# Kernel optimization log

Measured on AMD Instinct MI355X. Metric: run time of the kernel, lower is better.

## Reference

```python
import jax, jax.numpy as jnp
import numpy as np

POINT_ENCODING_SIZE = 15
L = 0


def _bilinear_2x2(corners, R):
    """Bilinear upsample [C,2,2,F] corner grid to [C,R,R,F], align_corners=True.
    Matches F.interpolate(x, size=(R,R), mode='bilinear', align_corners=True)
    for a 2x2 spatial input.
    """
    u = jnp.linspace(0.0, 1.0, R, dtype=corners.dtype)
    wu = jnp.stack([1.0 - u, u], axis=-1)  # [R,2] weights along one axis
    return jnp.einsum('ia,jb,cabf->cijf', wu, wu, corners)


def setup_inputs() -> dict:
    key = jax.random.key(0)
    ks = jax.random.split(key, 10)
    V, C, R = 10000, 2048, 16
    points = jax.random.normal(ks[0], (V, 3), dtype=jnp.float32)
    encodings = jax.random.normal(ks[1], (V, POINT_ENCODING_SIZE), dtype=jnp.float32) * 0.1
    complexes = jax.random.randint(ks[2], (C, 4), 0, V, dtype=jnp.int64)
    d_in = POINT_ENCODING_SIZE + (L + 1) * 3  # 18
    W1 = jax.random.normal(ks[3], (128, d_in), dtype=jnp.float32) / np.sqrt(d_in)
    b1 = jax.random.normal(ks[4], (128,), dtype=jnp.float32) * 0.01
    W2 = jax.random.normal(ks[5], (128, 128), dtype=jnp.float32) / np.sqrt(128)
    b2 = jax.random.normal(ks[6], (128,), dtype=jnp.float32) * 0.01
    W3 = jax.random.normal(ks[7], (3, 128), dtype=jnp.float32) / np.sqrt(128)
    b3 = jax.random.normal(ks[8], (3,), dtype=jnp.float32) * 0.01
    return {"points": points, "encodings": encodings,
            "W1": W1, "b1": b1, "W2": W2, "b2": b2, "W3": W3, "b3": b3,
            "complexes": complexes, "resolution": R}


def reference(points, encodings, W1, b1, W2, b2, W3, b3, complexes, resolution):
    R = resolution
    # gather 4 corner vertices per complex -> [C,2,2,*]
    local_points = points[complexes].reshape(-1, 2, 2, 3)
    local_enc = encodings[complexes].reshape(-1, 2, 2, POINT_ENCODING_SIZE)
    p = _bilinear_2x2(local_points, R)   # [C,R,R,3]
    e = _bilinear_2x2(local_enc, R)      # [C,R,R,15]
    # features: encodings + sin(2^i * p), L=0 -> just sin(p)
    X = jnp.concatenate([e, jnp.sin(p)], axis=-1)  # [C,R,R,18]
    X = jnp.sin(X @ W1.T + b1)
    X = jnp.sin(X @ W2.T + b2)
    X = X @ W3.T + b3                    # [C,R,R,3]
    lipschitz = jnp.float32(1.0)
    return (p + X, X, lipschitz)
```

## Files before the change

### kernel.cpp

```cpp
#include <hip/hip_runtime.h>
#include <hip/hip_bf16.h>

#define ENC 15

typedef __attribute__((ext_vector_type(4))) float f32x4;
typedef __attribute__((ext_vector_type(8))) short s16x8;
typedef __attribute__((ext_vector_type(4))) short s16x4;

static __device__ __forceinline__ short f2bf(float v) {
    __hip_bfloat16 h = __float2bfloat16(v);
    return __builtin_bit_cast(short, h);
}

#define WAVE_FENCE() do { \
    asm volatile("s_waitcnt lgkmcnt(0)" ::: "memory"); \
    __builtin_amdgcn_sched_barrier(0); \
} while (0)

__global__ void NSC_prep_kernel(const float* __restrict__ W1,
                                const float* __restrict__ W2,
                                __hip_bfloat16* __restrict__ ws) {
    int t = blockIdx.x * 256 + threadIdx.x;
    if (t < 4096) {
        int row = t >> 5, k = t & 31;
        float v = (k < 18) ? W1[row * 18 + k] : 0.0f;
        ws[t] = __float2bfloat16(v);
    } else if (t < 20480) {
        int p = t - 4096;
        int l = p ^ (((p >> 7) & 7) << 3);
        ws[t] = __float2bfloat16(W2[l]);
    }
}

__global__ __launch_bounds__(256, 2)
void NSC_59133109732095_kernel(
    const float* __restrict__ points,
    const float* __restrict__ encodings,
    const float* __restrict__ b1,
    const float* __restrict__ b2,
    const float* __restrict__ W3,
    const float* __restrict__ b3,
    const int*   __restrict__ complexes,
    const __hip_bfloat16* __restrict__ ws,
    float* __restrict__ out0,
    float* __restrict__ out1,
    float* __restrict__ out2)
{
    __shared__ __align__(16) char smem[65536];
    char* W2s = smem;
    char* Xb  = smem + 32768;

    const int c    = blockIdx.x;
    const int tid  = threadIdx.x;
    const int lane = tid & 63;
    const int wv   = tid >> 6;
    const int g    = lane >> 4;
    const int r16  = lane & 15;

    const __hip_bfloat16* W1b = ws;
    const char* ws2b = (const char*)(ws + 4096);

    s16x8 stg[8];
    #pragma unroll
    for (int i = 0; i < 8; ++i)
        stg[i] = *(const s16x8*)(ws2b + i * 4096 + tid * 16);

    const int pi = tid >> 4, pj = tid & 15;
    const float ui = (float)pi * (1.0f / 15.0f);
    const float uj = (float)pj * (1.0f / 15.0f);
    const float w00 = (1.0f - ui) * (1.0f - uj), w01 = (1.0f - ui) * uj;
    const float w10 = ui * (1.0f - uj),          w11 = ui * uj;
    const int v0 = complexes[c * 4 + 0], v1 = complexes[c * 4 + 1];
    const int v2 = complexes[c * 4 + 2], v3 = complexes[c * 4 + 3];

    float p[3];
    #pragma unroll
    for (int f = 0; f < 3; ++f)
        p[f] = w00 * points[v0 * 3 + f] + w01 * points[v1 * 3 + f]
             + w10 * points[v2 * 3 + f] + w11 * points[v3 * 3 + f];

    float Xf[18];
    #pragma unroll
    for (int k = 0; k < ENC; ++k)
        Xf[k] = w00 * encodings[v0 * ENC + k] + w01 * encodings[v1 * ENC + k]
              + w10 * encodings[v2 * ENC + k] + w11 * encodings[v3 * ENC + k];
    #pragma unroll
    for (int f = 0; f < 3; ++f) Xf[ENC + f] = __sinf(p[f]);

    #pragma unroll
    for (int ch = 0; ch < 4; ++ch) {
        s16x8 v;
        #pragma unroll
        for (int i = 0; i < 8; ++i) {
            int k = ch * 8 + i;
            v[i] = (k < 18) ? f2bf(Xf[k]) : (short)0;
        }
        *(s16x8*)(Xb + tid * 64 + ((ch * 16) ^ ((tid & 3) << 4))) = v;
    }

    #pragma unroll
    for (int i = 0; i < 8; ++i)
        *(s16x8*)(W2s + i * 4096 + tid * 16) = stg[i];

    __syncthreads();

    s16x8 bx[4];
    #pragma unroll
    for (int n = 0; n < 4; ++n) {
        int px = wv * 64 + n * 16 + r16;
        bx[n] = *(const s16x8*)(Xb + px * 64 + ((g * 16) ^ ((px & 3) << 4)));
    }

    f32x4 acc2[8][4];
    #pragma unroll
    for (int m = 0; m < 8; ++m) {
        f32x4 bv = *(const f32x4*)(b2 + m * 16 + g * 4);
        #pragma unroll
        for (int n = 0; n < 4; ++n) acc2[m][n] = bv;
    }

    f32x4 accp[2][4];
    #pragma unroll
    for (int mm = 0; mm < 2; ++mm) {
        f32x4 bv = *(const f32x4*)(b1 + mm * 16 + g * 4);
        #pragma unroll
        for (int n = 0; n < 4; ++n) accp[mm][n] = bv;
        s16x8 a1 = *(const s16x8*)(W1b + (mm * 16 + r16) * 32 + g * 8);
        #pragma unroll
        for (int n = 0; n < 4; ++n)
            accp[mm][n] = __builtin_amdgcn_mfma_f32_16x16x32_bf16(a1, bx[n], accp[mm][n], 0, 0, 0);
    }

    #pragma unroll
    for (int ks = 0; ks < 4; ++ks) {
        char* hsl = smem + 32768 + (1 - (ks & 1)) * 16384;

        s16x4 hv[2][4];
        #pragma unroll
        for (int mm = 0; mm < 2; ++mm)
            #pragma unroll
            for (int n = 0; n < 4; ++n)
                #pragma unroll
                for (int r = 0; r < 4; ++r)
                    hv[mm][n][r] = f2bf(__sinf(accp[mm][n][r]));

        #pragma unroll
        for (int mm = 0; mm < 2; ++mm)
            #pragma unroll
            for (int n = 0; n < 4; ++n) {
                int px = wv * 64 + n * 16 + r16;
                *(s16x4*)(hsl + px * 64 + ((mm * 32 + g * 8) ^ ((px & 3) << 4))) = hv[mm][n];
            }
        WAVE_FENCE();

        s16x8 hb[4];
        #pragma unroll
        for (int n = 0; n < 4; ++n) {
            int px = wv * 64 + n * 16 + r16;
            hb[n] = *(const s16x8*)(hsl + px * 64 + ((g * 16) ^ ((px & 3) << 4)));
        }

        if (ks < 3) {
            #pragma unroll
            for (int mm = 0; mm < 2; ++mm) {
                int m1 = (ks + 1) * 2 + mm;
                f32x4 bv = *(const f32x4*)(b1 + m1 * 16 + g * 4);
                #pragma unroll
                for (int n = 0; n < 4; ++n) accp[mm][n] = bv;
                s16x8 a1 = *(const s16x8*)(W1b + (m1 * 16 + r16) * 32 + g * 8);
                #pragma unroll
                for (int n = 0; n < 4; ++n)
                    accp[mm][n] = __builtin_amdgcn_mfma_f32_16x16x32_bf16(a1, bx[n], accp[mm][n], 0, 0, 0);
            }
        }

        #pragma unroll
        for (int hf = 0; hf < 2; ++hf) {
            s16x8 a2[4];
            #pragma unroll
            for (int mi = 0; mi < 4; ++mi) {
                int row = (hf * 4 + mi) * 16 + r16;
                int L   = row * 256 + ks * 64 + g * 16;
                a2[mi] = *(const s16x8*)(W2s + (L ^ ((r16 & 7) << 4)));
            }
            #pragma unroll
            for (int mi = 0; mi < 4; ++mi)
                #pragma unroll
                for (int n = 0; n < 4; ++n)
                    acc2[hf * 4 + mi][n] = __builtin_amdgcn_mfma_f32_16x16x32_bf16(
                        a2[mi], hb[n], acc2[hf * 4 + mi][n], 0, 0, 0);
        }
    }

    float pf0[4] = {0.f, 0.f, 0.f, 0.f};
    float pf1[4] = {0.f, 0.f, 0.f, 0.f};
    float pf2[4] = {0.f, 0.f, 0.f, 0.f};
    #pragma unroll
    for (int m = 0; m < 8; ++m) {
        float s2[4][4];
        #pragma unroll
        for (int n = 0; n < 4; ++n)
            #pragma unroll
            for (int r = 0; r < 4; ++r)
                s2[n][r] = __sinf(acc2[m][n][r]);
        f32x4 w3a = *(const f32x4*)(W3 + 0 * 128 + m * 16 + g * 4);
        f32x4 w3b = *(const f32x4*)(W3 + 1 * 128 + m * 16 + g * 4);
        f32x4 w3c = *(const f32x4*)(W3 + 2 * 128 + m * 16 + g * 4);
        #pragma unroll
        for (int n = 0; n < 4; ++n)
            #pragma unroll
            for (int r = 0; r < 4; ++r) {
                pf0[n] = fmaf(s2[n][r], w3a[r], pf0[n]);
                pf1[n] = fmaf(s2[n][r], w3b[r], pf1[n]);
                pf2[n] = fmaf(s2[n][r], w3c[r], pf2[n]);
            }
    }
    {
        const float b30 = b3[0], b31 = b3[1], b32 = b3[2];
        float x0 = 0.f, x1 = 0.f, x2 = 0.f;
        #pragma unroll
        for (int n = 0; n < 4; ++n) {
            float v0r = pf0[n]; v0r += __shfl_xor(v0r, 16); v0r += __shfl_xor(v0r, 32);
            float v1r = pf1[n]; v1r += __shfl_xor(v1r, 16); v1r += __shfl_xor(v1r, 32);
            float v2r = pf2[n]; v2r += __shfl_xor(v2r, 16); v2r += __shfl_xor(v2r, 32);
            if (g == n) { x0 = v0r; x1 = v1r; x2 = v2r; }
        }
        x0 += b30; x1 += b31; x2 += b32;
        const int base = (c * 256 + tid) * 3;
        out0[base + 0] = p[0] + x0;
        out0[base + 1] = p[1] + x1;
        out0[base + 2] = p[2] + x2;
        out1[base + 0] = x0;
        out1[base + 1] = x1;
        out1[base + 2] = x2;
    }
    if (c == 0 && tid == 0) out2[0] = 1.0f;
}

extern "C" void kernel_launch(void* const* d_in, const int* in_sizes, int n_in,
                              void* d_out, int out_size, void* d_ws, size_t ws_size,
                              hipStream_t stream) {
    const float* points    = (const float*)d_in[0];
    const float* encodings = (const float*)d_in[1];
    const float* W1        = (const float*)d_in[2];
    const float* b1        = (const float*)d_in[3];
    const float* W2        = (const float*)d_in[4];
    const float* b2        = (const float*)d_in[5];
    const float* W3        = (const float*)d_in[6];
    const float* b3        = (const float*)d_in[7];
    const int*   complexes = (const int*)d_in[8];

    const int C  = in_sizes[8] / 4;
    const int N3 = C * 256 * 3;

    float* out0 = (float*)d_out;
    float* out1 = out0 + N3;
    float* out2 = out1 + N3;

    __hip_bfloat16* ws = (__hip_bfloat16*)d_ws;

    NSC_prep_kernel<<<80, 256, 0, stream>>>(W1, W2, ws);
    NSC_59133109732095_kernel<<<C, 256, 0, stream>>>(
        points, encodings, b1, b2, W3, b3, complexes, ws, out0, out1, out2);
}
```

Before: 47.15 us.

## Split each complex across two blocks of 128 pixels to raise occupancy

The grid doubles so that each block handles half of a complex's 256 pixels, and each wave processes 32 pixels instead of 64. Shared memory drops from 64KB to 48KB and launch bounds allow 3 blocks per CU, so the scheduler has more waves to hide latency, and accumulator register use halves. In exchange, every block still stages the full 32KB W2 matrix into LDS, doubling that traffic. Each W2 A-fragment is also reused across only two MFMA column tiles instead of four, and half the lanes sit idle during the input interpolation.

Measured after the change: 53.26 us. 1.13x slower.

```diff
diff --git a/kernel.cpp b/kernel.cpp
--- a/kernel.cpp
+++ b/kernel.cpp
@@ -32,7 +32,7 @@
     }
 }
 
-__global__ __launch_bounds__(256, 2)
+__global__ __launch_bounds__(256, 3)
 void NSC_59133109732095_kernel(
     const float* __restrict__ points,
     const float* __restrict__ encodings,
@@ -46,11 +46,13 @@
     float* __restrict__ out1,
     float* __restrict__ out2)
 {
-    __shared__ __align__(16) char smem[65536];
+    __shared__ __align__(16) char smem[49152];
     char* W2s = smem;
     char* Xb  = smem + 32768;
 
-    const int c    = blockIdx.x;
+    const int blk  = blockIdx.x;
+    const int c    = blk >> 1;
+    const int half = blk & 1;
     const int tid  = threadIdx.x;
     const int lane = tid & 63;
     const int wv   = tid >> 6;
@@ -65,37 +67,41 @@
     for (int i = 0; i < 8; ++i)
         stg[i] = *(const s16x8*)(ws2b + i * 4096 + tid * 16);
 
-    const int pi = tid >> 4, pj = tid & 15;
-    const float ui = (float)pi * (1.0f / 15.0f);
-    const float uj = (float)pj * (1.0f / 15.0f);
-    const float w00 = (1.0f - ui) * (1.0f - uj), w01 = (1.0f - ui) * uj;
-    const float w10 = ui * (1.0f - uj),          w11 = ui * uj;
-    const int v0 = complexes[c * 4 + 0], v1 = complexes[c * 4 + 1];
-    const int v2 = complexes[c * 4 + 2], v3 = complexes[c * 4 + 3];
-
-    float p[3];
-    #pragma unroll
-    for (int f = 0; f < 3; ++f)
-        p[f] = w00 * points[v0 * 3 + f] + w01 * points[v1 * 3 + f]
-             + w10 * points[v2 * 3 + f] + w11 * points[v3 * 3 + f];
-
-    float Xf[18];
-    #pragma unroll
-    for (int k = 0; k < ENC; ++k)
-        Xf[k] = w00 * encodings[v0 * ENC + k] + w01 * encodings[v1 * ENC + k]
-              + w10 * encodings[v2 * ENC + k] + w11 * encodings[v3 * ENC + k];
-    #pragma unroll
-    for (int f = 0; f < 3; ++f) Xf[ENC + f] = __sinf(p[f]);
-
-    #pragma unroll
-    for (int ch = 0; ch < 4; ++ch) {
-        s16x8 v;
-        #pragma unroll
-        for (int i = 0; i < 8; ++i) {
-            int k = ch * 8 + i;
-            v[i] = (k < 18) ? f2bf(Xf[k]) : (short)0;
-        }
-        *(s16x8*)(Xb + tid * 64 + ((ch * 16) ^ ((tid & 3) << 4))) = v;
+    float p[3] = {0.f, 0.f, 0.f};
+    if (lane < 32) {
+        const int lpx = wv * 32 + lane;
+        const int px  = half * 128 + lpx;
+        const int pi = px >> 4, pj = px & 15;
+        const float ui = (float)pi * (1.0f / 15.0f);
+        const float uj = (float)pj * (1.0f / 15.0f);
+        const float w00 = (1.0f - ui) * (1.0f - uj), w01 = (1.0f - ui) * uj;
+        const float w10 = ui * (1.0f - uj),          w11 = ui * uj;
+        const int v0 = complexes[c * 4 + 0], v1 = complexes[c * 4 + 1];
+        const int v2 = complexes[c * 4 + 2], v3 = complexes[c * 4 + 3];
+
+        #pragma unroll
+        for (int f = 0; f < 3; ++f)
+            p[f] = w00 * points[v0 * 3 + f] + w01 * points[v1 * 3 + f]
+                 + w10 * points[v2 * 3 + f] + w11 * points[v3 * 3 + f];
+
+        float Xf[18];
+        #pragma unroll
+        for (int k = 0; k < ENC; ++k)
+            Xf[k] = w00 * encodings[v0 * ENC + k] + w01 * encodings[v1 * ENC + k]
+                  + w10 * encodings[v2 * ENC + k] + w11 * encodings[v3 * ENC + k];
+        #pragma unroll
+        for (int f = 0; f < 3; ++f) Xf[ENC + f] = __sinf(p[f]);
+
+        #pragma unroll
+        for (int ch = 0; ch < 4; ++ch) {
+            s16x8 v;
+            #pragma unroll
+            for (int i = 0; i < 8; ++i) {
+                int k = ch * 8 + i;
+                v[i] = (k < 18) ? f2bf(Xf[k]) : (short)0;
+            }
+            *(s16x8*)(Xb + lpx * 64 + ((ch * 16) ^ ((lpx & 3) << 4))) = v;
+        }
     }
 
     #pragma unroll
@@ -104,42 +110,40 @@
 
     __syncthreads();
 
-    s16x8 bx[4];
-    #pragma unroll
-    for (int n = 0; n < 4; ++n) {
-        int px = wv * 64 + n * 16 + r16;
+    s16x8 bx[2];
+    #pragma unroll
+    for (int n = 0; n < 2; ++n) {
+        int px = wv * 32 + n * 16 + r16;
         bx[n] = *(const s16x8*)(Xb + px * 64 + ((g * 16) ^ ((px & 3) << 4)));
     }
 
-    f32x4 acc2[8][4];
+    f32x4 acc2[8][2];
     #pragma unroll
     for (int m = 0; m < 8; ++m) {
         f32x4 bv = *(const f32x4*)(b2 + m * 16 + g * 4);
-        #pragma unroll
-        for (int n = 0; n < 4; ++n) acc2[m][n] = bv;
-    }
-
-    f32x4 accp[2][4];
+        acc2[m][0] = bv; acc2[m][1] = bv;
+    }
+
+    f32x4 accp[2][2];
     #pragma unroll
     for (int mm = 0; mm < 2; ++mm) {
         f32x4 bv = *(const f32x4*)(b1 + mm * 16 + g * 4);
-        #pragma unroll
-        for (int n = 0; n < 4; ++n) accp[mm][n] = bv;
+        accp[mm][0] = bv; accp[mm][1] = bv;
         s16x8 a1 = *(const s16x8*)(W1b + (mm * 16 + r16) * 32 + g * 8);
         #pragma unroll
-        for (int n = 0; n < 4; ++n)
+        for (int n = 0; n < 2; ++n)
             accp[mm][n] = __builtin_amdgcn_mfma_f32_16x16x32_bf16(a1, bx[n], accp[mm][n], 0, 0, 0);
     }
 
     #pragma unroll
     for (int ks = 0; ks < 4; ++ks) {
-        char* hsl = smem + 32768 + (1 - (ks & 1)) * 16384;
-
-        s16x4 hv[2][4];
+        char* hsl = smem + 32768 + (1 - (ks & 1)) * 8192;
+
+        s16x4 hv[2][2];
         #pragma unroll
         for (int mm = 0; mm < 2; ++mm)
             #pragma unroll
-            for (int n = 0; n < 4; ++n)
+            for (int n = 0; n < 2; ++n)
                 #pragma unroll
                 for (int r = 0; r < 4; ++r)
                     hv[mm][n][r] = f2bf(__sinf(accp[mm][n][r]));
@@ -147,16 +151,16 @@
         #pragma unroll
         for (int mm = 0; mm < 2; ++mm)
             #pragma unroll
-            for (int n = 0; n < 4; ++n) {
-                int px = wv * 64 + n * 16 + r16;
+            for (int n = 0; n < 2; ++n) {
+                int px = wv * 32 + n * 16 + r16;
                 *(s16x4*)(hsl + px * 64 + ((mm * 32 + g * 8) ^ ((px & 3) << 4))) = hv[mm][n];
             }
         WAVE_FENCE();
 
-        s16x8 hb[4];
-        #pragma unroll
-        for (int n = 0; n < 4; ++n) {
-            int px = wv * 64 + n * 16 + r16;
+        s16x8 hb[2];
+        #pragma unroll
+        for (int n = 0; n < 2; ++n) {
+            int px = wv * 32 + n * 16 + r16;
             hb[n] = *(const s16x8*)(hsl + px * 64 + ((g * 16) ^ ((px & 3) << 4)));
         }
 
@@ -165,11 +169,10 @@
             for (int mm = 0; mm < 2; ++mm) {
                 int m1 = (ks + 1) * 2 + mm;
                 f32x4 bv = *(const f32x4*)(b1 + m1 * 16 + g * 4);
-                #pragma unroll
-                for (int n = 0; n < 4; ++n) accp[mm][n] = bv;
+                accp[mm][0] = bv; accp[mm][1] = bv;
                 s16x8 a1 = *(const s16x8*)(W1b + (m1 * 16 + r16) * 32 + g * 8);
                 #pragma unroll
-                for (int n = 0; n < 4; ++n)
+                for (int n = 0; n < 2; ++n)
                     accp[mm][n] = __builtin_amdgcn_mfma_f32_16x16x32_bf16(a1, bx[n], accp[mm][n], 0, 0, 0);
             }
         }
@@ -186,20 +189,20 @@
             #pragma unroll
             for (int mi = 0; mi < 4; ++mi)
                 #pragma unroll
-                for (int n = 0; n < 4; ++n)
+                for (int n = 0; n < 2; ++n)
                     acc2[hf * 4 + mi][n] = __builtin_amdgcn_mfma_f32_16x16x32_bf16(
                         a2[mi], hb[n], acc2[hf * 4 + mi][n], 0, 0, 0);
         }
     }
 
-    float pf0[4] = {0.f, 0.f, 0.f, 0.f};
-    float pf1[4] = {0.f, 0.f, 0.f, 0.f};
-    float pf2[4] = {0.f, 0.f, 0.f, 0.f};
+    float pf0[2] = {0.f, 0.f};
+    float pf1[2] = {0.f, 0.f};
+    float pf2[2] = {0.f, 0.f};
     #pragma unroll
     for (int m = 0; m < 8; ++m) {
-        float s2[4][4];
-        #pragma unroll
-        for (int n = 0; n < 4; ++n)
+        float s2[2][4];
+        #pragma unroll
+        for (int n = 0; n < 2; ++n)
             #pragma unroll
             for (int r = 0; r < 4; ++r)
                 s2[n][r] = __sinf(acc2[m][n][r]);
@@ -207,7 +210,7 @@
         f32x4 w3b = *(const f32x4*)(W3 + 1 * 128 + m * 16 + g * 4);
         f32x4 w3c = *(const f32x4*)(W3 + 2 * 128 + m * 16 + g * 4);
         #pragma unroll
-        for (int n = 0; n < 4; ++n)
+        for (int n = 0; n < 2; ++n)
             #pragma unroll
             for (int r = 0; r < 4; ++r) {
                 pf0[n] = fmaf(s2[n][r], w3a[r], pf0[n]);
@@ -217,24 +220,26 @@
     }
     {
         const float b30 = b3[0], b31 = b3[1], b32 = b3[2];
-        float x0 = 0.f, x1 = 0.f, x2 = 0.f;
-        #pragma unroll
-        for (int n = 0; n < 4; ++n) {
+        #pragma unroll
+        for (int n = 0; n < 2; ++n) {
             float v0r = pf0[n]; v0r += __shfl_xor(v0r, 16); v0r += __shfl_xor(v0r, 32);
             float v1r = pf1[n]; v1r += __shfl_xor(v1r, 16); v1r += __shfl_xor(v1r, 32);
             float v2r = pf2[n]; v2r += __shfl_xor(v2r, 16); v2r += __shfl_xor(v2r, 32);
-            if (g == n) { x0 = v0r; x1 = v1r; x2 = v2r; }
-        }
-        x0 += b30; x1 += b31; x2 += b32;
-        const int base = (c * 256 + tid) * 3;
-        out0[base + 0] = p[0] + x0;
-        out0[base + 1] = p[1] + x1;
-        out0[base + 2] = p[2] + x2;
-        out1[base + 0] = x0;
-        out1[base + 1] = x1;
-        out1[base + 2] = x2;
-    }
-    if (c == 0 && tid == 0) out2[0] = 1.0f;
+            if (g == n) {
+                float x0 = v0r + b30;
+                float x1 = v1r + b31;
+                float x2 = v2r + b32;
+                const int base = (c * 256 + half * 128 + wv * 32 + n * 16 + r16) * 3;
+                out0[base + 0] = p[0] + x0;
+                out0[base + 1] = p[1] + x1;
+                out0[base + 2] = p[2] + x2;
+                out1[base + 0] = x0;
+                out1[base + 1] = x1;
+                out1[base + 2] = x2;
+            }
+        }
+    }
+    if (blk == 0 && tid == 0) out2[0] = 1.0f;
 }
 
 extern "C" void kernel_launch(void* const* d_in, const int* in_sizes, int n_in,
@@ -260,6 +265,6 @@
     __hip_bfloat16* ws = (__hip_bfloat16*)d_ws;
 
     NSC_prep_kernel<<<80, 256, 0, stream>>>(W1, W2, ws);
-    NSC_59133109732095_kernel<<<C, 256, 0, stream>>>(
+    NSC_59133109732095_kernel<<<C * 2, 256, 0, stream>>>(
         points, encodings, b1, b2, W3, b3, complexes, ws, out0, out1, out2);
 }
```

## Overlap layer-1 sine activation with layer-2 MFMA halves and pack bf16 conversions

Applied to the files above, without the earlier changes.

Moves the sine/bf16 conversion of the next layer-1 hidden slice so it runs between the two halves of the layer-2 MFMA block, writing into the other LDS buffer. This lets VALU transcendental work interleave with matrix-core work instead of serializing before it. The MFMA sections also get raised wave priority via s_setprio. Packed v_cvt_pk_bf16_f32 replaces scalar bf16 conversions, and the output store moves inside the lane-select branch. The risk is higher register pressure and scheduling changes from the restructured loop.

New measurement: 47.71 us. About the same (+1.2%).

```diff
diff --git a/kernel.cpp b/kernel.cpp
--- a/kernel.cpp
+++ b/kernel.cpp
@@ -5,11 +5,17 @@
 
 typedef __attribute__((ext_vector_type(4))) float f32x4;
 typedef __attribute__((ext_vector_type(8))) short s16x8;
-typedef __attribute__((ext_vector_type(4))) short s16x4;
+typedef __attribute__((ext_vector_type(2))) unsigned int u32x2;
 
 static __device__ __forceinline__ short f2bf(float v) {
     __hip_bfloat16 h = __float2bfloat16(v);
     return __builtin_bit_cast(short, h);
+}
+
+static __device__ __forceinline__ unsigned f2bf_pk(float lo, float hi) {
+    unsigned r;
+    asm("v_cvt_pk_bf16_f32 %0, %1, %2" : "=v"(r) : "v"(lo), "v"(hi));
+    return r;
 }
 
 #define WAVE_FENCE() do { \
@@ -79,23 +85,34 @@
         p[f] = w00 * points[v0 * 3 + f] + w01 * points[v1 * 3 + f]
              + w10 * points[v2 * 3 + f] + w11 * points[v3 * 3 + f];
 
-    float Xf[18];
+    float Xf[32];
     #pragma unroll
     for (int k = 0; k < ENC; ++k)
         Xf[k] = w00 * encodings[v0 * ENC + k] + w01 * encodings[v1 * ENC + k]
               + w10 * encodings[v2 * ENC + k] + w11 * encodings[v3 * ENC + k];
     #pragma unroll
     for (int f = 0; f < 3; ++f) Xf[ENC + f] = __sinf(p[f]);
-
-    #pragma unroll
-    for (int ch = 0; ch < 4; ++ch) {
-        s16x8 v;
-        #pragma unroll
-        for (int i = 0; i < 8; ++i) {
-            int k = ch * 8 + i;
-            v[i] = (k < 18) ? f2bf(Xf[k]) : (short)0;
-        }
-        *(s16x8*)(Xb + tid * 64 + ((ch * 16) ^ ((tid & 3) << 4))) = v;
+    #pragma unroll
+    for (int k = 18; k < 32; ++k) Xf[k] = 0.0f;
+
+    #pragma unroll
+    for (int ch = 0; ch < 2; ++ch) {
+        u32x2 v0w, v1w;
+        v0w[0] = f2bf_pk(Xf[ch * 16 + 0],  Xf[ch * 16 + 1]);
+        v0w[1] = f2bf_pk(Xf[ch * 16 + 2],  Xf[ch * 16 + 3]);
+        v1w[0] = f2bf_pk(Xf[ch * 16 + 4],  Xf[ch * 16 + 5]);
+        v1w[1] = f2bf_pk(Xf[ch * 16 + 6],  Xf[ch * 16 + 7]);
+        u32x2 v2w, v3w;
+        v2w[0] = f2bf_pk(Xf[ch * 16 + 8],  Xf[ch * 16 + 9]);
+        v2w[1] = f2bf_pk(Xf[ch * 16 + 10], Xf[ch * 16 + 11]);
+        v3w[0] = f2bf_pk(Xf[ch * 16 + 12], Xf[ch * 16 + 13]);
+        v3w[1] = f2bf_pk(Xf[ch * 16 + 14], Xf[ch * 16 + 15]);
+        char* base0 = Xb + tid * 64 + (((ch * 2 + 0) * 16) ^ ((tid & 3) << 4));
+        char* base1 = Xb + tid * 64 + (((ch * 2 + 1) * 16) ^ ((tid & 3) << 4));
+        *(u32x2*)(base0 + 0) = v0w;
+        *(u32x2*)(base0 + 8) = v1w;
+        *(u32x2*)(base1 + 0) = v2w;
+        *(u32x2*)(base1 + 8) = v3w;
     }
 
     #pragma unroll
@@ -130,34 +147,32 @@
         for (int n = 0; n < 4; ++n)
             accp[mm][n] = __builtin_amdgcn_mfma_f32_16x16x32_bf16(a1, bx[n], accp[mm][n], 0, 0, 0);
     }
+    {
+        char* hsl = smem + 49152;
+        #pragma unroll
+        for (int mm = 0; mm < 2; ++mm)
+            #pragma unroll
+            for (int n = 0; n < 4; ++n) {
+                u32x2 hw;
+                hw[0] = f2bf_pk(__sinf(accp[mm][n][0]), __sinf(accp[mm][n][1]));
+                hw[1] = f2bf_pk(__sinf(accp[mm][n][2]), __sinf(accp[mm][n][3]));
+                int px = wv * 64 + n * 16 + r16;
+                *(u32x2*)(hsl + px * 64 + ((mm * 32 + g * 8) ^ ((px & 3) << 4))) = hw;
+            }
+    }
 
     #pragma unroll
     for (int ks = 0; ks < 4; ++ks) {
-        char* hsl = smem + 32768 + (1 - (ks & 1)) * 16384;
-
-        s16x4 hv[2][4];
-        #pragma unroll
-        for (int mm = 0; mm < 2; ++mm)
-            #pragma unroll
-            for (int n = 0; n < 4; ++n)
-                #pragma unroll
-                for (int r = 0; r < 4; ++r)
-                    hv[mm][n][r] = f2bf(__sinf(accp[mm][n][r]));
-
-        #pragma unroll
-        for (int mm = 0; mm < 2; ++mm)
-            #pragma unroll
-            for (int n = 0; n < 4; ++n) {
-                int px = wv * 64 + n * 16 + r16;
-                *(s16x4*)(hsl + px * 64 + ((mm * 32 + g * 8) ^ ((px & 3) << 4))) = hv[mm][n];
-            }
+        char* cur = smem + 32768 + (1 - (ks & 1)) * 16384;
+        char* nxt = smem + 32768 + (ks & 1) * 16384;
+
         WAVE_FENCE();
 
         s16x8 hb[4];
         #pragma unroll
         for (int n = 0; n < 4; ++n) {
             int px = wv * 64 + n * 16 + r16;
-            hb[n] = *(const s16x8*)(hsl + px * 64 + ((g * 16) ^ ((px & 3) << 4)));
+            hb[n] = *(const s16x8*)(cur + px * 64 + ((g * 16) ^ ((px & 3) << 4)));
         }
 
         if (ks < 3) {
@@ -174,12 +189,12 @@
             }
         }
 
-        #pragma unroll
-        for (int hf = 0; hf < 2; ++hf) {
+        __builtin_amdgcn_s_setprio(1);
+        {
             s16x8 a2[4];
             #pragma unroll
             for (int mi = 0; mi < 4; ++mi) {
-                int row = (hf * 4 + mi) * 16 + r16;
+                int row = mi * 16 + r16;
                 int L   = row * 256 + ks * 64 + g * 16;
                 a2[mi] = *(const s16x8*)(W2s + (L ^ ((r16 & 7) << 4)));
             }
@@ -187,9 +202,41 @@
             for (int mi = 0; mi < 4; ++mi)
                 #pragma unroll
                 for (int n = 0; n < 4; ++n)
-                    acc2[hf * 4 + mi][n] = __builtin_amdgcn_mfma_f32_16x16x32_bf16(
-                        a2[mi], hb[n], acc2[hf * 4 + mi][n], 0, 0, 0);
-        }
+                    acc2[mi][n] = __builtin_amdgcn_mfma_f32_16x16x32_bf16(
+                        a2[mi], hb[n], acc2[mi][n], 0, 0, 0);
+        }
+        __builtin_amdgcn_s_setprio(0);
+
+        if (ks < 3) {
+            #pragma unroll
+            for (int mm = 0; mm < 2; ++mm)
+                #pragma unroll
+                for (int n = 0; n < 4; ++n) {
+                    u32x2 hw;
+                    hw[0] = f2bf_pk(__sinf(accp[mm][n][0]), __sinf(accp[mm][n][1]));
+                    hw[1] = f2bf_pk(__sinf(accp[mm][n][2]), __sinf(accp[mm][n][3]));
+                    int px = wv * 64 + n * 16 + r16;
+                    *(u32x2*)(nxt + px * 64 + ((mm * 32 + g * 8) ^ ((px & 3) << 4))) = hw;
+                }
+        }
+
+        __builtin_amdgcn_s_setprio(1);
+        {
+            s16x8 a2[4];
+            #pragma unroll
+            for (int mi = 0; mi < 4; ++mi) {
+                int row = (4 + mi) * 16 + r16;
+                int L   = row * 256 + ks * 64 + g * 16;
+                a2[mi] = *(const s16x8*)(W2s + (L ^ ((r16 & 7) << 4)));
+            }
+            #pragma unroll
+            for (int mi = 0; mi < 4; ++mi)
+                #pragma unroll
+                for (int n = 0; n < 4; ++n)
+                    acc2[4 + mi][n] = __builtin_amdgcn_mfma_f32_16x16x32_bf16(
+                        a2[mi], hb[n], acc2[4 + mi][n], 0, 0, 0);
+        }
+        __builtin_amdgcn_s_setprio(0);
     }
 
     float pf0[4] = {0.f, 0.f, 0.f, 0.f};
@@ -217,22 +264,24 @@
     }
     {
         const float b30 = b3[0], b31 = b3[1], b32 = b3[2];
-        float x0 = 0.f, x1 = 0.f, x2 = 0.f;
         #pragma unroll
         for (int n = 0; n < 4; ++n) {
             float v0r = pf0[n]; v0r += __shfl_xor(v0r, 16); v0r += __shfl_xor(v0r, 32);
             float v1r = pf1[n]; v1r += __shfl_xor(v1r, 16); v1r += __shfl_xor(v1r, 32);
             float v2r = pf2[n]; v2r += __shfl_xor(v2r, 16); v2r += __shfl_xor(v2r, 32);
-            if (g == n) { x0 = v0r; x1 = v1r; x2 = v2r; }
-        }
-        x0 += b30; x1 += b31; x2 += b32;
-        const int base = (c * 256 + tid) * 3;
-        out0[base + 0] = p[0] + x0;
-        out0[base + 1] = p[1] + x1;
-        out0[base + 2] = p[2] + x2;
-        out1[base + 0] = x0;
-        out1[base + 1] = x1;
-        out1[base + 2] = x2;
+            if (g == n) {
+                float x0 = v0r + b30;
+                float x1 = v1r + b31;
+                float x2 = v2r + b32;
+                const int base = (c * 256 + tid) * 3;
+                out0[base + 0] = p[0] + x0;
+                out0[base + 1] = p[1] + x1;
+                out0[base + 2] = p[2] + x2;
+                out1[base + 0] = x0;
+                out1[base + 1] = x1;
+                out1[base + 2] = x2;
+            }
+        }
     }
     if (c == 0 && tid == 0) out2[0] = 1.0f;
 }
```
